# Optimization experiments

Measured on AMD Instinct MI355X. Metric: run time of the kernel, lower is better.

Reference implementation:

```python
import jax, jax.numpy as jnp
import numpy as np

N_NODES = 50000
N_EDGES = 600000
F_IN = 128
HID = 128
N_CLASSES = 10
N_GRAPHS = 64


def _glorot(key, shape):
    fan_in, fan_out = shape[1], shape[0]
    lim = float(np.sqrt(6.0 / (fan_in + fan_out)))
    return jax.random.uniform(key, shape, jnp.float32, -lim, lim)


def setup_inputs() -> dict:
    key = jax.random.key(0)
    ks = jax.random.split(key, 16)
    x = jax.random.normal(ks[0], (N_NODES, F_IN), jnp.float32)
    edge_index = jax.random.randint(ks[1], (2, N_EDGES), 0, N_NODES, jnp.int64)
    batch = jnp.sort(jax.random.randint(ks[2], (N_NODES,), 0, N_GRAPHS, jnp.int64))
    # GraphConv params: lin_rel (with bias) applied to aggregated neighbor sum,
    # lin_root (no bias) applied to the node's own features.
    params = dict(
        W1_rel=_glorot(ks[3], (HID, F_IN)), b1_rel=jnp.zeros((HID,), jnp.float32),
        W1_root=_glorot(ks[4], (HID, F_IN)),
        W2_rel=_glorot(ks[5], (HID, HID)), b2_rel=jnp.zeros((HID,), jnp.float32),
        W2_root=_glorot(ks[6], (HID, HID)),
        W3_rel=_glorot(ks[7], (HID, HID)), b3_rel=jnp.zeros((HID,), jnp.float32),
        W3_root=_glorot(ks[8], (HID, HID)),
        W_lin=_glorot(ks[9], (N_CLASSES, HID)), b_lin=jnp.zeros((N_CLASSES,), jnp.float32),
    )
    return {"x": x, "edge_index": edge_index, "batch": batch, **params}


def _graph_conv(x, src, dst, W_rel, b_rel, W_root):
    # gather source features, scatter-add into targets, then linear (sum aggr
    # commutes with the linear, matching PyG GraphConv which applies lin_rel
    # after aggregation)
    agg = jax.ops.segment_sum(x[src], dst, num_segments=N_NODES)  # [N, F]
    return agg @ W_rel.T + b_rel + x @ W_root.T


def _mean_pool(x, batch):
    sums = jax.ops.segment_sum(x, batch, num_segments=N_GRAPHS)  # [G, H]
    cnts = jax.ops.segment_sum(jnp.ones((x.shape[0],), x.dtype), batch,
                               num_segments=N_GRAPHS)
    return sums / jnp.maximum(cnts, 1.0)[:, None]


def reference(x, edge_index, batch,
              W1_rel, b1_rel, W1_root,
              W2_rel, b2_rel, W2_root,
              W3_rel, b3_rel, W3_root,
              W_lin, b_lin):
    src, dst = edge_index[0], edge_index[1]
    h = jax.nn.relu(_graph_conv(x, src, dst, W1_rel, b1_rel, W1_root))
    h = jax.nn.relu(_graph_conv(h, src, dst, W2_rel, b2_rel, W2_root))
    h = _graph_conv(h, src, dst, W3_rel, b3_rel, W3_root)
    g = _mean_pool(h, batch)  # [G, H]
    # dropout is identity in eval mode (training=False)
    return g @ W_lin.T + b_lin  # [G, num_classes]
```

## Files before the change

kernel.cpp:

```cpp
#include <hip/hip_runtime.h>
#include <hip/hip_bf16.h>

#define N_NODES   50000
#define N_EDGES   600000
#define F         128
#define N_GRAPHS  64
#define N_CLASSES 10
#define NPAD      50048
#define MAXDEG    64
#define XCVT_BLOCKS 6250
#define WCVT_BLOCKS 96
#define EDGE_BLOCKS 2344

typedef __attribute__((ext_vector_type(8))) short bf16x8;
typedef __attribute__((ext_vector_type(4))) float f32x4;

static __device__ __forceinline__ unsigned short f2bf(float f) {
    __hip_bfloat16 h = __float2bfloat16(f);
    return *reinterpret_cast<unsigned short*>(&h);
}
static __device__ __forceinline__ float bf2f(unsigned short u) {
    return __uint_as_float(((unsigned)u) << 16);
}

__global__ __launch_bounds__(256) void prep_kernel(
    const float* __restrict__ x,
    const float* __restrict__ W0, const float* __restrict__ W1,
    const float* __restrict__ W2, const float* __restrict__ W3,
    const float* __restrict__ W4, const float* __restrict__ W5,
    const int* __restrict__ src, const int* __restrict__ dst,
    unsigned short* __restrict__ Xb, unsigned short* __restrict__ Wb,
    int* __restrict__ deg, int* __restrict__ csrF)
{
    int b = blockIdx.x;
    if (b < XCVT_BLOCKS) {
        int i = b * 256 + threadIdx.x;
        float4 v = reinterpret_cast<const float4*>(x)[i];
        ushort4 o;
        o.x = f2bf(v.x); o.y = f2bf(v.y); o.z = f2bf(v.z); o.w = f2bf(v.w);
        reinterpret_cast<ushort4*>(Xb)[i] = o;
    } else if (b < XCVT_BLOCKS + WCVT_BLOCKS) {
        const int PER = (F * F / 4) / 256;
        int bb  = b - XCVT_BLOCKS;
        int mat = bb / PER;
        int i   = (bb % PER) * 256 + threadIdx.x;
        const float* W = (mat == 0) ? W0 : (mat == 1) ? W1 : (mat == 2) ? W2
                       : (mat == 3) ? W3 : (mat == 4) ? W4 : W5;
        float4 v = reinterpret_cast<const float4*>(W)[i];
        ushort4 o;
        o.x = f2bf(v.x); o.y = f2bf(v.y); o.z = f2bf(v.z); o.w = f2bf(v.w);
        reinterpret_cast<ushort4*>(Wb + (size_t)mat * F * F)[i] = o;
    } else {
        int e = (b - XCVT_BLOCKS - WCVT_BLOCKS) * 256 + threadIdx.x;
        if (e < N_EDGES) {
            int d = dst[e];
            int slot = atomicAdd(&deg[d], 1);
            if (slot < MAXDEG) csrF[d * MAXDEG + slot] = src[e];
        }
    }
}

template <int RELU>
__global__ __launch_bounds__(256) void conv_fused(
    const unsigned short* __restrict__ Xb,
    const int* __restrict__ deg, const int* __restrict__ csrF,
    const unsigned short* __restrict__ Wrel, const unsigned short* __restrict__ Wroot,
    const float* __restrict__ brel, unsigned short* __restrict__ H)
{
    __shared__ char AsRaw[64 * 256];
    const int t = threadIdx.x;
    const int mBase = blockIdx.x * 64;

    {
        const int r = t >> 2;
        const int q = t & 3;
        int row = mBase + r;
        float acc[32];
#pragma unroll
        for (int i = 0; i < 32; ++i) acc[i] = 0.f;
        if (row < N_NODES) {
            int n = deg[row];
            if (n > MAXDEG) n = MAXDEG;
            const int* lst = csrF + row * MAXDEG;
            const unsigned short* Xq = Xb + (size_t)q * 32;
            int j = 0;
            for (; j + 2 <= n; j += 2) {
                int sa = lst[j], sb = lst[j + 1];
                const bf16x8* pa = reinterpret_cast<const bf16x8*>(Xq + (size_t)sa * F);
                const bf16x8* pb = reinterpret_cast<const bf16x8*>(Xq + (size_t)sb * F);
                bf16x8 va0 = pa[0], va1 = pa[1], va2 = pa[2], va3 = pa[3];
                bf16x8 vb0 = pb[0], vb1 = pb[1], vb2 = pb[2], vb3 = pb[3];
#pragma unroll
                for (int e = 0; e < 8; ++e) {
                    acc[e]      += bf2f((unsigned short)va0[e]) + bf2f((unsigned short)vb0[e]);
                    acc[8 + e]  += bf2f((unsigned short)va1[e]) + bf2f((unsigned short)vb1[e]);
                    acc[16 + e] += bf2f((unsigned short)va2[e]) + bf2f((unsigned short)vb2[e]);
                    acc[24 + e] += bf2f((unsigned short)va3[e]) + bf2f((unsigned short)vb3[e]);
                }
            }
            if (j < n) {
                int sa = lst[j];
                const bf16x8* pa = reinterpret_cast<const bf16x8*>(Xq + (size_t)sa * F);
                bf16x8 va0 = pa[0], va1 = pa[1], va2 = pa[2], va3 = pa[3];
#pragma unroll
                for (int e = 0; e < 8; ++e) {
                    acc[e]      += bf2f((unsigned short)va0[e]);
                    acc[8 + e]  += bf2f((unsigned short)va1[e]);
                    acc[16 + e] += bf2f((unsigned short)va2[e]);
                    acc[24 + e] += bf2f((unsigned short)va3[e]);
                }
            }
        }
#pragma unroll
        for (int cc = 0; cc < 4; ++cc) {
            bf16x8 o;
#pragma unroll
            for (int e = 0; e < 8; ++e) o[e] = (short)f2bf(acc[cc * 8 + e]);
            int bytecol = (q * 64 + cc * 16) ^ ((r & 7) << 4);
            *reinterpret_cast<bf16x8*>(AsRaw + r * 256 + bytecol) = o;
        }
    }
    __syncthreads();

    const int wave = t >> 6;
    const int lane = t & 63;
    const int wm = wave >> 1, wn = wave & 1;
    const int m0l = wm * 32;
    const int n0  = wn * 64;
    const int lrow = lane & 15;
    const int lk8  = (lane >> 4) << 3;

    f32x4 acc[2][4];
#pragma unroll
    for (int mi = 0; mi < 2; ++mi)
#pragma unroll
        for (int ni = 0; ni < 4; ++ni)
            acc[mi][ni] = (f32x4){0.f, 0.f, 0.f, 0.f};

#pragma unroll
    for (int p = 0; p < 2; ++p) {
        const unsigned short* W = p ? Wroot : Wrel;
#pragma unroll
        for (int ks = 0; ks < 4; ++ks) {
            int k0 = ks * 32 + lk8;
            bf16x8 a[2], b[4];
#pragma unroll
            for (int mi = 0; mi < 2; ++mi) {
                int rl = m0l + mi * 16 + lrow;
                if (p == 0) {
                    int bytecol = (k0 * 2) ^ ((rl & 7) << 4);
                    a[mi] = *reinterpret_cast<const bf16x8*>(AsRaw + rl * 256 + bytecol);
                } else {
                    a[mi] = *reinterpret_cast<const bf16x8*>(
                        Xb + (size_t)(mBase + rl) * F + k0);
                }
            }
#pragma unroll
            for (int ni = 0; ni < 4; ++ni)
                b[ni] = *reinterpret_cast<const bf16x8*>(
                    W + (size_t)(n0 + ni * 16 + lrow) * F + k0);
#pragma unroll
            for (int mi = 0; mi < 2; ++mi)
#pragma unroll
                for (int ni = 0; ni < 4; ++ni)
                    acc[mi][ni] = __builtin_amdgcn_mfma_f32_16x16x32_bf16(
                        a[mi], b[ni], acc[mi][ni], 0, 0, 0);
        }
    }

    const int r0 = (lane >> 4) << 2;
#pragma unroll
    for (int ni = 0; ni < 4; ++ni) {
        int col = n0 + ni * 16 + lrow;
        float bb = brel[col];
#pragma unroll
        for (int mi = 0; mi < 2; ++mi) {
#pragma unroll
            for (int r = 0; r < 4; ++r) {
                int row = mBase + m0l + mi * 16 + r0 + r;
                if (row < N_NODES) {
                    float v = acc[mi][ni][r] + bb;
                    if (RELU) v = fmaxf(v, 0.f);
                    H[(size_t)row * F + col] = f2bf(v);
                }
            }
        }
    }
}

__global__ __launch_bounds__(256) void poolhead_kernel(
    const unsigned short* __restrict__ H, const int* __restrict__ batch,
    const float* __restrict__ Wl, const float* __restrict__ bl,
    float* __restrict__ out)
{
    int g = blockIdx.x;
    int lo = 0, hi = N_NODES;
    while (lo < hi) { int m = (lo + hi) >> 1; if (batch[m] < g) lo = m + 1; else hi = m; }
    int start = lo;
    hi = N_NODES;
    while (lo < hi) { int m = (lo + hi) >> 1; if (batch[m] < g + 1) lo = m + 1; else hi = m; }
    int end = lo;

    int l8 = (threadIdx.x & 15) << 3;
    int rg = threadIdx.x >> 4;
    float acc[8] = {0.f, 0.f, 0.f, 0.f, 0.f, 0.f, 0.f, 0.f};
    for (int i = start + rg; i < end; i += 16) {
        bf16x8 v = *reinterpret_cast<const bf16x8*>(H + (size_t)i * F + l8);
#pragma unroll
        for (int r = 0; r < 8; ++r) acc[r] += bf2f((unsigned short)v[r]);
    }
    __shared__ float sh[16][F];
    __shared__ float mean[F];
#pragma unroll
    for (int r = 0; r < 8; ++r) sh[rg][l8 + r] = acc[r];
    __syncthreads();
    if (threadIdx.x < F) {
        int f = threadIdx.x;
        float s = 0.f;
#pragma unroll
        for (int k = 0; k < 16; ++k) s += sh[k][f];
        float cnt = (float)(end - start);
        mean[f] = s / fmaxf(cnt, 1.f);
    }
    __syncthreads();
    if (threadIdx.x < N_CLASSES) {
        int c = threadIdx.x;
        float s = bl[c];
#pragma unroll 8
        for (int k = 0; k < F; ++k) s += mean[k] * Wl[c * F + k];
        out[g * N_CLASSES + c] = s;
    }
}

extern "C" void kernel_launch(void* const* d_in, const int* in_sizes, int n_in,
                              void* d_out, int out_size, void* d_ws, size_t ws_size,
                              hipStream_t stream)
{
    const float* x     = (const float*)d_in[0];
    const int*   edge  = (const int*)d_in[1];
    const int*   src   = edge;
    const int*   dst   = edge + N_EDGES;
    const int*   batch = (const int*)d_in[2];
    const float* W1r = (const float*)d_in[3];
    const float* b1  = (const float*)d_in[4];
    const float* W1o = (const float*)d_in[5];
    const float* W2r = (const float*)d_in[6];
    const float* b2  = (const float*)d_in[7];
    const float* W2o = (const float*)d_in[8];
    const float* W3r = (const float*)d_in[9];
    const float* b3  = (const float*)d_in[10];
    const float* W3o = (const float*)d_in[11];
    const float* Wl  = (const float*)d_in[12];
    const float* bl  = (const float*)d_in[13];
    float* out = (float*)d_out;

    char* ws = (char*)d_ws;
    const size_t fb = (size_t)NPAD * F * sizeof(unsigned short);
    unsigned short* Xb  = (unsigned short*)ws;
    unsigned short* H1b = (unsigned short*)(ws + fb);
    unsigned short* H2b = (unsigned short*)(ws + 2 * fb);
    char* p = ws + 3 * fb;
    unsigned short* Wb = (unsigned short*)p;
    p += (size_t)6 * F * F * sizeof(unsigned short);
    int* deg  = (int*)p;                 p += (size_t)N_NODES * sizeof(int);
    int* csrF = (int*)p;                 p += (size_t)N_NODES * MAXDEG * sizeof(int);

    const int convBlocks = NPAD / 64;
    const int prepBlocks = XCVT_BLOCKS + WCVT_BLOCKS + EDGE_BLOCKS;

    hipMemsetAsync(deg, 0, (size_t)N_NODES * sizeof(int), stream);
    prep_kernel<<<prepBlocks, 256, 0, stream>>>(x, W1r, W1o, W2r, W2o, W3r, W3o,
                                                src, dst, Xb, Wb, deg, csrF);

    conv_fused<1><<<convBlocks, 256, 0, stream>>>(Xb,  deg, csrF, Wb + 0 * F * F, Wb + 1 * F * F, b1, H1b);
    conv_fused<1><<<convBlocks, 256, 0, stream>>>(H1b, deg, csrF, Wb + 2 * F * F, Wb + 3 * F * F, b2, H2b);
    conv_fused<0><<<convBlocks, 256, 0, stream>>>(H2b, deg, csrF, Wb + 4 * F * F, Wb + 5 * F * F, b3, H1b);

    poolhead_kernel<<<N_GRAPHS, 256, 0, stream>>>(H1b, batch, Wl, bl, out);
}
```

Before: 250.1 us.

## Narrow neighbor indices to 16-bit and regroup gather lanes per row

Neighbor lists are now stored as unsigned short instead of int. This is valid because the node count is below 65536, and it halves the size of the adjacency buffer and its read traffic. The aggregation phase changes its mapping: 16 lanes now share one node, each lane reading 16 bytes of the neighbor's feature row so that the full 256-byte row is fetched in one coalesced access. Each thread loops over 4 nodes and unrolls up to 8 neighbor loads at a time to keep more memory requests in flight. In exchange, each thread handles its nodes serially, and the index narrowing only holds while the node count stays below 65536.

```diff
diff --git a/kernel.cpp b/kernel.cpp
--- a/kernel.cpp
+++ b/kernel.cpp
@@ -30,7 +30,7 @@
     const float* __restrict__ W4, const float* __restrict__ W5,
     const int* __restrict__ src, const int* __restrict__ dst,
     unsigned short* __restrict__ Xb, unsigned short* __restrict__ Wb,
-    int* __restrict__ deg, int* __restrict__ csrF)
+    int* __restrict__ deg, unsigned short* __restrict__ csrF)
 {
     int b = blockIdx.x;
     if (b < XCVT_BLOCKS) {
@@ -55,7 +55,8 @@
         if (e < N_EDGES) {
             int d = dst[e];
             int slot = atomicAdd(&deg[d], 1);
-            if (slot < MAXDEG) csrF[d * MAXDEG + slot] = src[e];
+            if (slot < MAXDEG)
+                csrF[(size_t)d * MAXDEG + slot] = (unsigned short)src[e];
         }
     }
 }
@@ -63,7 +64,7 @@
 template <int RELU>
 __global__ __launch_bounds__(256) void conv_fused(
     const unsigned short* __restrict__ Xb,
-    const int* __restrict__ deg, const int* __restrict__ csrF,
+    const int* __restrict__ deg, const unsigned short* __restrict__ csrF,
     const unsigned short* __restrict__ Wrel, const unsigned short* __restrict__ Wroot,
     const float* __restrict__ brel, unsigned short* __restrict__ H)
 {
@@ -72,51 +73,59 @@
     const int mBase = blockIdx.x * 64;
 
     {
-        const int r = t >> 2;
-        const int q = t & 3;
-        int row = mBase + r;
-        float acc[32];
-#pragma unroll
-        for (int i = 0; i < 32; ++i) acc[i] = 0.f;
-        if (row < N_NODES) {
-            int n = deg[row];
-            if (n > MAXDEG) n = MAXDEG;
-            const int* lst = csrF + row * MAXDEG;
-            const unsigned short* Xq = Xb + (size_t)q * 32;
-            int j = 0;
-            for (; j + 2 <= n; j += 2) {
-                int sa = lst[j], sb = lst[j + 1];
-                const bf16x8* pa = reinterpret_cast<const bf16x8*>(Xq + (size_t)sa * F);
-                const bf16x8* pb = reinterpret_cast<const bf16x8*>(Xq + (size_t)sb * F);
-                bf16x8 va0 = pa[0], va1 = pa[1], va2 = pa[2], va3 = pa[3];
-                bf16x8 vb0 = pb[0], vb1 = pb[1], vb2 = pb[2], vb3 = pb[3];
-#pragma unroll
-                for (int e = 0; e < 8; ++e) {
-                    acc[e]      += bf2f((unsigned short)va0[e]) + bf2f((unsigned short)vb0[e]);
-                    acc[8 + e]  += bf2f((unsigned short)va1[e]) + bf2f((unsigned short)vb1[e]);
-                    acc[16 + e] += bf2f((unsigned short)va2[e]) + bf2f((unsigned short)vb2[e]);
-                    acc[24 + e] += bf2f((unsigned short)va3[e]) + bf2f((unsigned short)vb3[e]);
+        const int sub = t & 15;
+        const int rr  = t >> 4;
+        const unsigned short* Xq = Xb + sub * 8;
+#pragma unroll
+        for (int it = 0; it < 4; ++it) {
+            int r   = it * 16 + rr;
+            int row = mBase + r;
+            float acc[8] = {0.f, 0.f, 0.f, 0.f, 0.f, 0.f, 0.f, 0.f};
+            if (row < N_NODES) {
+                const unsigned short* lst = csrF + (size_t)row * MAXDEG;
+                int n = deg[row];
+                if (n > MAXDEG) n = MAXDEG;
+                int j = 0;
+                for (; j + 8 <= n; j += 8) {
+                    bf16x8 v[8];
+#pragma unroll
+                    for (int k = 0; k < 8; ++k)
+                        v[k] = *reinterpret_cast<const bf16x8*>(
+                            Xq + (size_t)lst[j + k] * F);
+#pragma unroll
+                    for (int e = 0; e < 8; ++e) {
+                        float s0 = bf2f((unsigned short)v[0][e]) + bf2f((unsigned short)v[1][e]);
+                        float s1 = bf2f((unsigned short)v[2][e]) + bf2f((unsigned short)v[3][e]);
+                        float s2 = bf2f((unsigned short)v[4][e]) + bf2f((unsigned short)v[5][e]);
+                        float s3 = bf2f((unsigned short)v[6][e]) + bf2f((unsigned short)v[7][e]);
+                        acc[e] += (s0 + s1) + (s2 + s3);
+                    }
+                }
+                if (j + 4 <= n) {
+                    bf16x8 v[4];
+#pragma unroll
+                    for (int k = 0; k < 4; ++k)
+                        v[k] = *reinterpret_cast<const bf16x8*>(
+                            Xq + (size_t)lst[j + k] * F);
+#pragma unroll
+                    for (int e = 0; e < 8; ++e) {
+                        float s0 = bf2f((unsigned short)v[0][e]) + bf2f((unsigned short)v[1][e]);
+                        float s1 = bf2f((unsigned short)v[2][e]) + bf2f((unsigned short)v[3][e]);
+                        acc[e] += s0 + s1;
+                    }
+                    j += 4;
+                }
+                for (; j < n; ++j) {
+                    bf16x8 v0 = *reinterpret_cast<const bf16x8*>(
+                        Xq + (size_t)lst[j] * F);
+#pragma unroll
+                    for (int e = 0; e < 8; ++e) acc[e] += bf2f((unsigned short)v0[e]);
                 }
             }
-            if (j < n) {
-                int sa = lst[j];
-                const bf16x8* pa = reinterpret_cast<const bf16x8*>(Xq + (size_t)sa * F);
-                bf16x8 va0 = pa[0], va1 = pa[1], va2 = pa[2], va3 = pa[3];
-#pragma unroll
-                for (int e = 0; e < 8; ++e) {
-                    acc[e]      += bf2f((unsigned short)va0[e]);
-                    acc[8 + e]  += bf2f((unsigned short)va1[e]);
-                    acc[16 + e] += bf2f((unsigned short)va2[e]);
-                    acc[24 + e] += bf2f((unsigned short)va3[e]);
-                }
-            }
-        }
-#pragma unroll
-        for (int cc = 0; cc < 4; ++cc) {
             bf16x8 o;
 #pragma unroll
-            for (int e = 0; e < 8; ++e) o[e] = (short)f2bf(acc[cc * 8 + e]);
-            int bytecol = (q * 64 + cc * 16) ^ ((r & 7) << 4);
+            for (int e = 0; e < 8; ++e) o[e] = (short)f2bf(acc[e]);
+            int bytecol = (sub * 16) ^ ((r & 7) << 4);
             *reinterpret_cast<bf16x8*>(AsRaw + r * 256 + bytecol) = o;
         }
     }
@@ -262,8 +271,9 @@
     char* p = ws + 3 * fb;
     unsigned short* Wb = (unsigned short*)p;
     p += (size_t)6 * F * F * sizeof(unsigned short);
-    int* deg  = (int*)p;                 p += (size_t)N_NODES * sizeof(int);
-    int* csrF = (int*)p;                 p += (size_t)N_NODES * MAXDEG * sizeof(int);
+    int* deg = (int*)p;                  p += (size_t)N_NODES * sizeof(int);
+    unsigned short* csrF = (unsigned short*)p;
+    p += (size_t)N_NODES * MAXDEG * sizeof(unsigned short);
 
     const int convBlocks = NPAD / 64;
     const int prepBlocks = XCVT_BLOCKS + WCVT_BLOCKS + EDGE_BLOCKS;
```

After: 220.6 us. 11.8% less time.
